# Kernel tuning notes

Measured on AMD Instinct MI355X. Metric: run time of the kernel, lower is better.

The kernel has to match this reference:

```python
import jax, jax.numpy as jnp
import numpy as np

B = 8192
N_MELS = 80
AUX = 32
RNN = 512
FC = 512
N_CLASSES = 512


def gru_cell(x, h, w_ih, w_hh, b_ih, b_hh):
    # torch.nn.GRUCell semantics; w_* are [3*H, in], gates ordered (r, z, n)
    gi = x @ w_ih.T + b_ih
    gh = h @ w_hh.T + b_hh
    i_r, i_z, i_n = jnp.split(gi, 3, axis=1)
    h_r, h_z, h_n = jnp.split(gh, 3, axis=1)
    r = jax.nn.sigmoid(i_r + h_r)
    z = jax.nn.sigmoid(i_z + h_z)
    n = jnp.tanh(i_n + r * h_n)
    return (1.0 - z) * n + z * h


def setup_inputs() -> dict:
    key = jax.random.key(0)
    ks = jax.random.split(key, 32)
    s = lambda k, shp, sc=0.05: (jax.random.normal(k, shp, dtype=jnp.float32) * sc)
    inp = {
        'm_t': jax.random.normal(ks[0], (B, N_MELS), dtype=jnp.float32),
        'a1_t': jax.random.normal(ks[1], (B, AUX), dtype=jnp.float32),
        'a2_t': jax.random.normal(ks[2], (B, AUX), dtype=jnp.float32),
        'a3_t': jax.random.normal(ks[3], (B, AUX), dtype=jnp.float32),
        'a4_t': jax.random.normal(ks[4], (B, AUX), dtype=jnp.float32),
        'h1': jax.random.normal(ks[5], (B, RNN), dtype=jnp.float32),
        'h2': jax.random.normal(ks[6], (B, RNN), dtype=jnp.float32),
        'x': jax.random.normal(ks[7], (B, 1), dtype=jnp.float32),
        # params
        'I_w': s(ks[8], (RNN, 1 + N_MELS + AUX)),
        'I_b': s(ks[9], (RNN,)),
        'rnn1_wih': s(ks[10], (3 * RNN, RNN)),
        'rnn1_whh': s(ks[11], (3 * RNN, RNN)),
        'rnn1_bih': s(ks[12], (3 * RNN,)),
        'rnn1_bhh': s(ks[13], (3 * RNN,)),
        'rnn2_wih': s(ks[14], (3 * RNN, RNN + AUX)),
        'rnn2_whh': s(ks[15], (3 * RNN, RNN)),
        'rnn2_bih': s(ks[16], (3 * RNN,)),
        'rnn2_bhh': s(ks[17], (3 * RNN,)),
        'fc1_w': s(ks[18], (FC, RNN + AUX)),
        'fc1_b': s(ks[19], (FC,)),
        'fc2_w': s(ks[20], (FC, FC + AUX)),
        'fc2_b': s(ks[21], (FC,)),
        'fc3_w': s(ks[22], (N_CLASSES, FC)),
        'fc3_b': s(ks[23], (N_CLASSES,)),
    }
    return inp


def reference(m_t, a1_t, a2_t, a3_t, a4_t, h1, h2, x,
              I_w, I_b, rnn1_wih, rnn1_whh, rnn1_bih, rnn1_bhh,
              rnn2_wih, rnn2_whh, rnn2_bih, rnn2_bhh,
              fc1_w, fc1_b, fc2_w, fc2_b, fc3_w, fc3_b):
    x = jnp.concatenate([x, m_t, a1_t], axis=1)
    x = x @ I_w.T + I_b
    h1n = gru_cell(x, h1, rnn1_wih, rnn1_whh, rnn1_bih, rnn1_bhh)
    x = x + h1n
    inp = jnp.concatenate([x, a2_t], axis=1)
    h2n = gru_cell(inp, h2, rnn2_wih, rnn2_whh, rnn2_bih, rnn2_bhh)
    x = x + h2n
    x = jnp.concatenate([x, a3_t], axis=1)
    x = jax.nn.relu(x @ fc1_w.T + fc1_b)
    x = jnp.concatenate([x, a4_t], axis=1)
    x = jax.nn.relu(x @ fc2_w.T + fc2_b)
    logits = x @ fc3_w.T + fc3_b
    return (logits, h1n, h2n)
```

## Files before the change

kernel.cpp:

```cpp
#include <hip/hip_runtime.h>


#define BK 32

typedef __attribute__((ext_vector_type(8))) short short8;
typedef __attribute__((ext_vector_type(4))) float f32x4;

__device__ __forceinline__ unsigned short f2bf(float f) {
    unsigned int u = __float_as_uint(f);
    u += 0x7fffu + ((u >> 16) & 1u);
    return (unsigned short)(u >> 16);
}
__device__ __forceinline__ float bf2f(unsigned short h) {
    return __uint_as_float(((unsigned int)h) << 16);
}
__device__ __forceinline__ float sigm(float x)  { return 1.f / (1.f + __expf(-x)); }
__device__ __forceinline__ float tanh_f(float x){ return 1.f - 2.f / (__expf(2.f * x) + 1.f); }

__device__ __forceinline__ void gl16(const void* g, void* l) {
    __builtin_amdgcn_global_load_lds(
        (const __attribute__((address_space(1))) unsigned int*)g,
        (__attribute__((address_space(3))) unsigned int*)l, 16, 0, 0);
}

struct GruArgs {
    const float* hprev;
    const float* xprev;
    float* hn_out;
    float* x_f32_out;
    unsigned short* x_bf_out;
    int out_stride;
};

__global__ __launch_bounds__(256)
void gru_k(const unsigned short* __restrict__ A1, const unsigned short* __restrict__ A2,
           const unsigned short* __restrict__ Wih, const unsigned short* __restrict__ Whh,
           const float* __restrict__ bih, const float* __restrict__ bhh,
           int kpad, GruArgs g)
{
    constexpr int BUFU = 32 * 512;
    __shared__ __align__(16) unsigned short lds[2 * BUFU];
    const int t    = threadIdx.x;
    const int m0   = blockIdx.x * 64;
    const int n0   = blockIdx.y * 64;
    const int lane = t & 63;
    const int w    = t >> 6;
    const int rl   = lane >> 2;
    const int cl   = (lane & 3) * 8;
    const int fr   = lane & 15;
    const int kg   = (lane >> 4) * 8;

    f32x4 acc[6][4] = {};
    const int NT = kpad >> 5;

    auto stage = [&](int buf, int k0) {
        unsigned short* dst = lds + buf * BUFU;
        const size_t rowoff = (size_t)(m0 + w * 16 + rl) * kpad + (k0 + cl);
        gl16(A1 + rowoff, dst + w * 512);
        gl16(A2 + rowoff, dst + (4 + w) * 512);
        #pragma unroll
        for (int j = 0; j < 6; ++j) {
            const unsigned short* Wp = (j < 3) ? Wih : Whh;
            const int s = (j < 3) ? j : j - 3;
            gl16(Wp + (size_t)(s * 512 + n0 + w * 16 + rl) * kpad + (k0 + cl),
                 dst + (8 + j * 4 + w) * 512);
        }
    };

    stage(0, 0);
    __syncthreads();
    int cur = 0;
    for (int tt = 0; tt < NT; ++tt) {
        if (tt + 1 < NT) stage(cur ^ 1, (tt + 1) * BK);
        const unsigned short* Bb = lds + cur * BUFU;
        short8 a1[4], a2[4];
        #pragma unroll
        for (int mi = 0; mi < 4; ++mi) {
            a1[mi] = *(const short8*)(Bb + (mi * 16 + fr) * 32 + kg);
            a2[mi] = *(const short8*)(Bb + 2048 + (mi * 16 + fr) * 32 + kg);
        }
        #pragma unroll
        for (int j = 0; j < 6; ++j) {
            short8 b = *(const short8*)(Bb + 4096 + j * 2048 + (w * 16 + fr) * 32 + kg);
            #pragma unroll
            for (int mi = 0; mi < 4; ++mi)
                acc[j][mi] = __builtin_amdgcn_mfma_f32_16x16x32_bf16(
                    (j < 3) ? a1[mi] : a2[mi], b, acc[j][mi], 0, 0, 0);
        }
        __syncthreads();
        cur ^= 1;
    }

    const int nn = n0 + w * 16 + fr;
    const float bir = bih[nn], biz = bih[512 + nn], bin_ = bih[1024 + nn];
    const float bhr = bhh[nn], bhz = bhh[512 + nn], bhn = bhh[1024 + nn];
    #pragma unroll
    for (int mi = 0; mi < 4; ++mi)
    #pragma unroll
    for (int v = 0; v < 4; ++v) {
        const int m = m0 + mi * 16 + (lane >> 4) * 4 + v;
        const size_t r0 = (size_t)m * 512;
        float r  = sigm(acc[0][mi][v] + bir + acc[3][mi][v] + bhr);
        float z  = sigm(acc[1][mi][v] + biz + acc[4][mi][v] + bhz);
        float nv = tanh_f(acc[2][mi][v] + bin_ + r * (acc[5][mi][v] + bhn));
        float h  = g.hprev[r0 + nn];
        float hv = (1.f - z) * nv + z * h;
        g.hn_out[r0 + nn] = hv;
        float xv = g.xprev[r0 + nn] + hv;
        if (g.x_f32_out) g.x_f32_out[r0 + nn] = xv;
        g.x_bf_out[(size_t)m * g.out_stride + nn] = f2bf(xv);
    }
}

struct EpiArgs { float* f32_out; unsigned short* bf_h; int out_stride; };

template<int EPI>
__global__ __launch_bounds__(256)
void gemm_k(const unsigned short* __restrict__ A, const unsigned short* __restrict__ W,
            const float* __restrict__ bias, int kpad, EpiArgs ea)
{
    constexpr int BUFU = 8 * 512;
    __shared__ __align__(16) unsigned short lds[2 * BUFU];
    const int t    = threadIdx.x;
    const int m0   = blockIdx.x * 64;
    const int n0   = blockIdx.y * 64;
    const int lane = t & 63;
    const int w    = t >> 6;
    const int rl   = lane >> 2;
    const int cl   = (lane & 3) * 8;
    const int fr   = lane & 15;
    const int kg   = (lane >> 4) * 8;

    f32x4 acc[4] = {};
    const int NT = kpad >> 5;

    auto stage = [&](int buf, int k0) {
        unsigned short* dst = lds + buf * BUFU;
        gl16(A + (size_t)(m0 + w * 16 + rl) * kpad + (k0 + cl), dst + w * 512);
        gl16(W + (size_t)(n0 + w * 16 + rl) * kpad + (k0 + cl), dst + (4 + w) * 512);
    };

    stage(0, 0);
    __syncthreads();
    int cur = 0;
    for (int tt = 0; tt < NT; ++tt) {
        if (tt + 1 < NT) stage(cur ^ 1, (tt + 1) * BK);
        const unsigned short* Bb = lds + cur * BUFU;
        short8 b = *(const short8*)(Bb + 2048 + (w * 16 + fr) * 32 + kg);
        #pragma unroll
        for (int mi = 0; mi < 4; ++mi) {
            short8 a = *(const short8*)(Bb + (mi * 16 + fr) * 32 + kg);
            acc[mi] = __builtin_amdgcn_mfma_f32_16x16x32_bf16(a, b, acc[mi], 0, 0, 0);
        }
        __syncthreads();
        cur ^= 1;
    }

    const int nn = n0 + w * 16 + fr;
    const float bv = bias[nn];
    #pragma unroll
    for (int mi = 0; mi < 4; ++mi)
    #pragma unroll
    for (int v = 0; v < 4; ++v) {
        const int m = m0 + mi * 16 + (lane >> 4) * 4 + v;
        float val = acc[mi][v] + bv;
        if constexpr (EPI == 0) {
            const size_t o = (size_t)m * 512 + nn;
            ea.f32_out[o] = val;
            ea.bf_h[o] = f2bf(val);
        } else if constexpr (EPI == 3) {
            val = fmaxf(val, 0.f);
            ea.bf_h[(size_t)m * ea.out_stride + nn] = f2bf(val);
        } else {
            ea.f32_out[(size_t)m * 512 + nn] = val;
        }
    }
}

struct SplitSeg { const float* src; unsigned short* dh; int K; int Kpad; int total; };
struct SplitArgs { SplitSeg seg[10]; };

__global__ void k_split(SplitArgs a) {
    const SplitSeg s = a.seg[blockIdx.y];
    const int stride = gridDim.x * blockDim.x;
    for (int i = blockIdx.x * blockDim.x + threadIdx.x; i < s.total; i += stride) {
        float v;
        if (s.K == s.Kpad) v = s.src[i];
        else {
            int row = i / s.Kpad;
            int col = i - row * s.Kpad;
            v = (col < s.K) ? s.src[(size_t)row * s.K + col] : 0.f;
        }
        s.dh[i] = f2bf(v);
    }
}

__global__ void k_build_c0(const float* __restrict__ x, const float* __restrict__ m,
                           const float* __restrict__ a1, unsigned short* __restrict__ dh) {
    int i = blockIdx.x * blockDim.x + threadIdx.x;
    int row = i >> 7, col = i & 127;
    float v = 0.f;
    if (col == 0)       v = x[row];
    else if (col < 81)  v = m[row * 80 + (col - 1)];
    else if (col < 113) v = a1[row * 32 + (col - 81)];
    dh[i] = f2bf(v);
}

__global__ void k_fill_tail(unsigned short* __restrict__ dh, const float* __restrict__ src) {
    int i = blockIdx.x * blockDim.x + threadIdx.x;
    int row = i >> 6, col = i & 63;
    float v = (col < 32) ? src[row * 32 + col] : 0.f;
    dh[(size_t)row * 576 + 512 + col] = f2bf(v);
}

extern "C" void kernel_launch(void* const* d_in, const int* in_sizes, int n_in,
                              void* d_out, int out_size, void* d_ws, size_t ws_size,
                              hipStream_t stream)
{
    const size_t OFF_WI   = 0;
    const size_t OFF_W1IH = 131072;
    const size_t OFF_W1HH = 1703936;
    const size_t OFF_W2IH = 3276800;
    const size_t OFF_W2HH = 5046272;
    const size_t OFF_WFC1 = 6815744;
    const size_t OFF_WFC2 = 7405568;
    const size_t OFF_WFC3 = 7995392;
    const size_t OFF_H1   = 8519680;
    const size_t OFF_H2   = 16908288;
    const size_t OFF_C0   = 26345472;
    const size_t OFF_X0H  = 28442624;
    const size_t OFF_X0F  = 36831232;
    const size_t OFF_X1F  = 53608448;
    const size_t OFF_X1C  = 70385664;
    const size_t OFF_X2C  = 79822848;
    const size_t OFF_X3C  = 89260032;
    const size_t OFF_X4   = 98697216;
    const size_t WS_NEEDED = 107085824;
    if (ws_size < WS_NEEDED) return;

    const float* m_t   = (const float*)d_in[0];
    const float* a1    = (const float*)d_in[1];
    const float* a2    = (const float*)d_in[2];
    const float* a3    = (const float*)d_in[3];
    const float* a4    = (const float*)d_in[4];
    const float* h1    = (const float*)d_in[5];
    const float* h2    = (const float*)d_in[6];
    const float* xin   = (const float*)d_in[7];
    const float* I_w   = (const float*)d_in[8];
    const float* I_b   = (const float*)d_in[9];
    const float* r1wih = (const float*)d_in[10];
    const float* r1whh = (const float*)d_in[11];
    const float* r1bih = (const float*)d_in[12];
    const float* r1bhh = (const float*)d_in[13];
    const float* r2wih = (const float*)d_in[14];
    const float* r2whh = (const float*)d_in[15];
    const float* r2bih = (const float*)d_in[16];
    const float* r2bhh = (const float*)d_in[17];
    const float* fc1w  = (const float*)d_in[18];
    const float* fc1b  = (const float*)d_in[19];
    const float* fc2w  = (const float*)d_in[20];
    const float* fc2b  = (const float*)d_in[21];
    const float* fc3w  = (const float*)d_in[22];
    const float* fc3b  = (const float*)d_in[23];
    float* out = (float*)d_out;

    char* ws = (char*)d_ws;
    auto U  = [&](size_t off) { return (unsigned short*)(ws + off); };
    auto Fp = [&](size_t off) { return (float*)(ws + off); };
    (void)in_sizes; (void)n_in; (void)out_size;

    SplitArgs sa;
    sa.seg[0] = { I_w,   U(OFF_WI),   113, 128, 512 * 128 };
    sa.seg[1] = { r1wih, U(OFF_W1IH), 512, 512, 1536 * 512 };
    sa.seg[2] = { r1whh, U(OFF_W1HH), 512, 512, 1536 * 512 };
    sa.seg[3] = { r2wih, U(OFF_W2IH), 544, 576, 1536 * 576 };
    sa.seg[4] = { r2whh, U(OFF_W2HH), 512, 576, 1536 * 576 };
    sa.seg[5] = { fc1w,  U(OFF_WFC1), 544, 576, 512 * 576 };
    sa.seg[6] = { fc2w,  U(OFF_WFC2), 544, 576, 512 * 576 };
    sa.seg[7] = { fc3w,  U(OFF_WFC3), 512, 512, 512 * 512 };
    sa.seg[8] = { h1,    U(OFF_H1),   512, 512, 8192 * 512 };
    sa.seg[9] = { h2,    U(OFF_H2),   512, 576, 8192 * 576 };
    hipLaunchKernelGGL(k_split, dim3(512, 10), dim3(256), 0, stream, sa);

    hipLaunchKernelGGL(k_build_c0, dim3(4096), dim3(256), 0, stream, xin, m_t, a1, U(OFF_C0));
    hipLaunchKernelGGL(k_fill_tail, dim3(2048), dim3(256), 0, stream, U(OFF_X1C), a2);
    hipLaunchKernelGGL(k_fill_tail, dim3(2048), dim3(256), 0, stream, U(OFF_X2C), a3);
    hipLaunchKernelGGL(k_fill_tail, dim3(2048), dim3(256), 0, stream, U(OFF_X3C), a4);

    EpiArgs ea{};
    ea.f32_out = Fp(OFF_X0F); ea.bf_h = U(OFF_X0H); ea.out_stride = 512;
    hipLaunchKernelGGL((gemm_k<0>), dim3(128, 8), dim3(256), 0, stream,
                       U(OFF_C0), U(OFF_WI), I_b, 128, ea);

    GruArgs g{};
    g.hprev = h1; g.xprev = Fp(OFF_X0F);
    g.hn_out = out + 4194304; g.x_f32_out = Fp(OFF_X1F);
    g.x_bf_out = U(OFF_X1C); g.out_stride = 576;
    hipLaunchKernelGGL(gru_k, dim3(128, 8), dim3(256), 0, stream,
                       U(OFF_X0H), U(OFF_H1), U(OFF_W1IH), U(OFF_W1HH), r1bih, r1bhh, 512, g);

    g = GruArgs{};
    g.hprev = h2; g.xprev = Fp(OFF_X1F);
    g.hn_out = out + 8388608; g.x_f32_out = nullptr;
    g.x_bf_out = U(OFF_X2C); g.out_stride = 576;
    hipLaunchKernelGGL(gru_k, dim3(128, 8), dim3(256), 0, stream,
                       U(OFF_X1C), U(OFF_H2), U(OFF_W2IH), U(OFF_W2HH), r2bih, r2bhh, 576, g);

    ea = EpiArgs{}; ea.bf_h = U(OFF_X3C); ea.out_stride = 576;
    hipLaunchKernelGGL((gemm_k<3>), dim3(128, 8), dim3(256), 0, stream,
                       U(OFF_X2C), U(OFF_WFC1), fc1b, 576, ea);
    ea = EpiArgs{}; ea.bf_h = U(OFF_X4); ea.out_stride = 512;
    hipLaunchKernelGGL((gemm_k<3>), dim3(128, 8), dim3(256), 0, stream,
                       U(OFF_X3C), U(OFF_WFC2), fc2b, 576, ea);
    ea = EpiArgs{}; ea.f32_out = out;
    hipLaunchKernelGGL((gemm_k<4>), dim3(128, 8), dim3(256), 0, stream,
                       U(OFF_X4), U(OFF_WFC3), fc3b, 512, ea);
}
```

Measured before the change: 337.0 us.

## Restructure GRU kernel into 128x64 tiles with split gi/gh warp groups

The GRU kernel now uses 512-thread blocks covering 128 rows by 64 columns. Four waves compute the input-gate products and four compute the hidden-gate products, each wave owning a 64x32 sub-tile. The hidden-gate accumulators are exchanged through LDS in two phases to finish the gate math, so each loaded weight tile feeds more rows and per-wave accumulator pressure drops. The cost is 80 KB of dynamic LDS, extra barriers in the epilogue, and lower occupancy. The fp32-to-bf16 split kernel is also vectorised to 8-element loads and stores for unpadded segments.

```diff
diff --git a/kernel.cpp b/kernel.cpp
--- a/kernel.cpp
+++ b/kernel.cpp
@@ -5,6 +5,7 @@
 
 typedef __attribute__((ext_vector_type(8))) short short8;
 typedef __attribute__((ext_vector_type(4))) float f32x4;
+typedef __attribute__((ext_vector_type(8))) unsigned short ush8;
 
 __device__ __forceinline__ unsigned short f2bf(float f) {
     unsigned int u = __float_as_uint(f);
@@ -32,38 +33,48 @@
     int out_stride;
 };
 
-__global__ __launch_bounds__(256)
+__global__ __launch_bounds__(512)
 void gru_k(const unsigned short* __restrict__ A1, const unsigned short* __restrict__ A2,
            const unsigned short* __restrict__ Wih, const unsigned short* __restrict__ Whh,
            const float* __restrict__ bih, const float* __restrict__ bhh,
            int kpad, GruArgs g)
 {
-    constexpr int BUFU = 32 * 512;
-    __shared__ __align__(16) unsigned short lds[2 * BUFU];
+    extern __shared__ __align__(16) unsigned short lds[];
+    constexpr int BUFU = 20480;
     const int t    = threadIdx.x;
-    const int m0   = blockIdx.x * 64;
+    const int w    = t >> 6;
+    const int lane = t & 63;
+    const int isgi = (w < 4);
+    const int ww   = w & 3;
+    const int mh   = ww >> 1;
+    const int nh   = ww & 1;
+    const int m0   = blockIdx.x * 128;
     const int n0   = blockIdx.y * 64;
-    const int lane = t & 63;
-    const int w    = t >> 6;
-    const int rl   = lane >> 2;
-    const int cl   = (lane & 3) * 8;
     const int fr   = lane & 15;
     const int kg   = (lane >> 4) * 8;
-
-    f32x4 acc[6][4] = {};
-    const int NT = kpad >> 5;
+    const int NT   = kpad >> 5;
+
+    f32x4 acc[3][4][2] = {};
 
     auto stage = [&](int buf, int k0) {
         unsigned short* dst = lds + buf * BUFU;
-        const size_t rowoff = (size_t)(m0 + w * 16 + rl) * kpad + (k0 + cl);
-        gl16(A1 + rowoff, dst + w * 512);
-        gl16(A2 + rowoff, dst + (4 + w) * 512);
-        #pragma unroll
-        for (int j = 0; j < 6; ++j) {
-            const unsigned short* Wp = (j < 3) ? Wih : Whh;
-            const int s = (j < 3) ? j : j - 3;
-            gl16(Wp + (size_t)(s * 512 + n0 + w * 16 + rl) * kpad + (k0 + cl),
-                 dst + (8 + j * 4 + w) * 512);
+        #pragma unroll
+        for (int k = 0; k < 5; ++k) {
+            const int u = k * 512 + w * 64 + lane;
+            const unsigned short* src;
+            if (u < 512) {
+                src = A1 + (size_t)(m0 + (u >> 2)) * kpad + k0 + (u & 3) * 8;
+            } else if (u < 1024) {
+                src = A2 + (size_t)(m0 + ((u - 512) >> 2)) * kpad + k0 + (u & 3) * 8;
+            } else {
+                const int v = u - 1024;
+                const int p = v >> 8;
+                const int r = (v & 255) >> 2;
+                const unsigned short* Wp = (p < 3) ? Wih : Whh;
+                const int s = (p < 3) ? p : p - 3;
+                src = Wp + (size_t)(s * 512 + n0 + r) * kpad + k0 + (u & 3) * 8;
+            }
+            gl16(src, dst + (size_t)(k * 512 + w * 64) * 8);
         }
     };
 
@@ -72,43 +83,88 @@
     int cur = 0;
     for (int tt = 0; tt < NT; ++tt) {
         if (tt + 1 < NT) stage(cur ^ 1, (tt + 1) * BK);
-        const unsigned short* Bb = lds + cur * BUFU;
-        short8 a1[4], a2[4];
-        #pragma unroll
-        for (int mi = 0; mi < 4; ++mi) {
-            a1[mi] = *(const short8*)(Bb + (mi * 16 + fr) * 32 + kg);
-            a2[mi] = *(const short8*)(Bb + 2048 + (mi * 16 + fr) * 32 + kg);
-        }
-        #pragma unroll
-        for (int j = 0; j < 6; ++j) {
-            short8 b = *(const short8*)(Bb + 4096 + j * 2048 + (w * 16 + fr) * 32 + kg);
+        const unsigned short* B0 = lds + cur * BUFU;
+        const unsigned short* Ab = B0 + (isgi ? 0 : 4096);
+        short8 a[4];
+        #pragma unroll
+        for (int mi = 0; mi < 4; ++mi)
+            a[mi] = *(const short8*)(Ab + (mh * 64 + mi * 16 + fr) * 32 + kg);
+        #pragma unroll
+        for (int s = 0; s < 3; ++s) {
+            const unsigned short* Bp = B0 + 8192 + (isgi ? s : s + 3) * 2048;
             #pragma unroll
-            for (int mi = 0; mi < 4; ++mi)
-                acc[j][mi] = __builtin_amdgcn_mfma_f32_16x16x32_bf16(
-                    (j < 3) ? a1[mi] : a2[mi], b, acc[j][mi], 0, 0, 0);
+            for (int ni = 0; ni < 2; ++ni) {
+                short8 b = *(const short8*)(Bp + (nh * 32 + ni * 16 + fr) * 32 + kg);
+                #pragma unroll
+                for (int mi = 0; mi < 4; ++mi)
+                    acc[s][mi][ni] = __builtin_amdgcn_mfma_f32_16x16x32_bf16(a[mi], b, acc[s][mi][ni], 0, 0, 0);
+            }
         }
         __syncthreads();
         cur ^= 1;
     }
 
-    const int nn = n0 + w * 16 + fr;
-    const float bir = bih[nn], biz = bih[512 + nn], bin_ = bih[1024 + nn];
-    const float bhr = bhh[nn], bhz = bhh[512 + nn], bhn = bhh[1024 + nn];
-    #pragma unroll
-    for (int mi = 0; mi < 4; ++mi)
-    #pragma unroll
-    for (int v = 0; v < 4; ++v) {
-        const int m = m0 + mi * 16 + (lane >> 4) * 4 + v;
-        const size_t r0 = (size_t)m * 512;
-        float r  = sigm(acc[0][mi][v] + bir + acc[3][mi][v] + bhr);
-        float z  = sigm(acc[1][mi][v] + biz + acc[4][mi][v] + bhz);
-        float nv = tanh_f(acc[2][mi][v] + bin_ + r * (acc[5][mi][v] + bhn));
-        float h  = g.hprev[r0 + nn];
-        float hv = (1.f - z) * nv + z * h;
-        g.hn_out[r0 + nn] = hv;
-        float xv = g.xprev[r0 + nn] + hv;
-        if (g.x_f32_out) g.x_f32_out[r0 + nn] = xv;
-        g.x_bf_out[(size_t)m * g.out_stride + nn] = f2bf(xv);
+    float* xf = (float*)lds;
+    if (!isgi) {
+        #pragma unroll
+        for (int s = 0; s < 2; ++s)
+        #pragma unroll
+        for (int mi = 0; mi < 4; ++mi)
+        #pragma unroll
+        for (int ni = 0; ni < 2; ++ni)
+            *(f32x4*)(xf + s * 8192 + ww * 2048 + (mi * 2 + ni) * 256 + lane * 4) = acc[s][mi][ni];
+    }
+    __syncthreads();
+    if (isgi) {
+        #pragma unroll
+        for (int mi = 0; mi < 4; ++mi)
+        #pragma unroll
+        for (int ni = 0; ni < 2; ++ni) {
+            const int nn = n0 + nh * 32 + ni * 16 + fr;
+            const float bir = bih[nn] + bhh[nn];
+            const float biz = bih[512 + nn] + bhh[512 + nn];
+            f32x4 ghr = *(const f32x4*)(xf + ww * 2048 + (mi * 2 + ni) * 256 + lane * 4);
+            f32x4 ghz = *(const f32x4*)(xf + 8192 + ww * 2048 + (mi * 2 + ni) * 256 + lane * 4);
+            #pragma unroll
+            for (int v = 0; v < 4; ++v) {
+                acc[0][mi][ni][v] = sigm(acc[0][mi][ni][v] + ghr[v] + bir);
+                acc[1][mi][ni][v] = sigm(acc[1][mi][ni][v] + ghz[v] + biz);
+            }
+        }
+    }
+    __syncthreads();
+    if (!isgi) {
+        #pragma unroll
+        for (int mi = 0; mi < 4; ++mi)
+        #pragma unroll
+        for (int ni = 0; ni < 2; ++ni)
+            *(f32x4*)(xf + ww * 2048 + (mi * 2 + ni) * 256 + lane * 4) = acc[2][mi][ni];
+    }
+    __syncthreads();
+    if (isgi) {
+        #pragma unroll
+        for (int mi = 0; mi < 4; ++mi)
+        #pragma unroll
+        for (int ni = 0; ni < 2; ++ni) {
+            const int nn = n0 + nh * 32 + ni * 16 + fr;
+            const float bin_ = bih[1024 + nn];
+            const float bhn  = bhh[1024 + nn];
+            f32x4 ghn = *(const f32x4*)(xf + ww * 2048 + (mi * 2 + ni) * 256 + lane * 4);
+            #pragma unroll
+            for (int v = 0; v < 4; ++v) {
+                const int m = m0 + mh * 64 + mi * 16 + (lane >> 4) * 4 + v;
+                const size_t r0 = (size_t)m * 512;
+                float r  = acc[0][mi][ni][v];
+                float z  = acc[1][mi][ni][v];
+                float nv = tanh_f(acc[2][mi][ni][v] + bin_ + r * (ghn[v] + bhn));
+                float h  = g.hprev[r0 + nn];
+                float hv = (1.f - z) * nv + z * h;
+                g.hn_out[r0 + nn] = hv;
+                float xv = g.xprev[r0 + nn] + hv;
+                if (g.x_f32_out) g.x_f32_out[r0 + nn] = xv;
+                g.x_bf_out[(size_t)m * g.out_stride + nn] = f2bf(xv);
+            }
+        }
     }
 }
 
@@ -183,15 +239,26 @@
 __global__ void k_split(SplitArgs a) {
     const SplitSeg s = a.seg[blockIdx.y];
     const int stride = gridDim.x * blockDim.x;
-    for (int i = blockIdx.x * blockDim.x + threadIdx.x; i < s.total; i += stride) {
-        float v;
-        if (s.K == s.Kpad) v = s.src[i];
-        else {
+    const int tid0 = blockIdx.x * blockDim.x + threadIdx.x;
+    if (s.K == s.Kpad) {
+        const int n8 = s.total >> 3;
+        const float4* src4 = (const float4*)s.src;
+        ush8* dst8 = (ush8*)s.dh;
+        for (int i = tid0; i < n8; i += stride) {
+            float4 f0 = src4[i * 2];
+            float4 f1 = src4[i * 2 + 1];
+            ush8 o;
+            o[0] = f2bf(f0.x); o[1] = f2bf(f0.y); o[2] = f2bf(f0.z); o[3] = f2bf(f0.w);
+            o[4] = f2bf(f1.x); o[5] = f2bf(f1.y); o[6] = f2bf(f1.z); o[7] = f2bf(f1.w);
+            dst8[i] = o;
+        }
+    } else {
+        for (int i = tid0; i < s.total; i += stride) {
             int row = i / s.Kpad;
             int col = i - row * s.Kpad;
-            v = (col < s.K) ? s.src[(size_t)row * s.K + col] : 0.f;
-        }
-        s.dh[i] = f2bf(v);
+            float v = (col < s.K) ? s.src[(size_t)row * s.K + col] : 0.f;
+            s.dh[i] = f2bf(v);
+        }
     }
 }
 
@@ -296,14 +363,14 @@
     g.hprev = h1; g.xprev = Fp(OFF_X0F);
     g.hn_out = out + 4194304; g.x_f32_out = Fp(OFF_X1F);
     g.x_bf_out = U(OFF_X1C); g.out_stride = 576;
-    hipLaunchKernelGGL(gru_k, dim3(128, 8), dim3(256), 0, stream,
+    hipLaunchKernelGGL(gru_k, dim3(64, 8), dim3(512), 81920, stream,
                        U(OFF_X0H), U(OFF_H1), U(OFF_W1IH), U(OFF_W1HH), r1bih, r1bhh, 512, g);
 
     g = GruArgs{};
     g.hprev = h2; g.xprev = Fp(OFF_X1F);
     g.hn_out = out + 8388608; g.x_f32_out = nullptr;
     g.x_bf_out = U(OFF_X2C); g.out_stride = 576;
-    hipLaunchKernelGGL(gru_k, dim3(128, 8), dim3(256), 0, stream,
+    hipLaunchKernelGGL(gru_k, dim3(64, 8), dim3(512), 81920, stream,
                        U(OFF_X1C), U(OFF_H2), U(OFF_W2IH), U(OFF_W2HH), r2bih, r2bhh, 576, g);
 
     ea = EpiArgs{}; ea.bf_h = U(OFF_X3C); ea.out_stride = 576;
```

New measurement: 326.7 us. 1.03x faster.
